# Kernel optimization log

Hardware: AMD Instinct MI355X
Metric: run time of the kernel (lower is better)

The kernel has to match this reference:

```python
import jax, jax.numpy as jnp
import numpy as np

K = 5
PAD = 2


def setup_inputs() -> dict:
    key = jax.random.key(0)
    k1, k2 = jax.random.split(key)
    B, C, H, W = 8, 4, 256, 256
    x = jax.random.normal(k1, (B, C, H, W), dtype=jnp.float32)
    filt = jax.random.uniform(k2, (B, C * K * K, H, W), dtype=jnp.float32)
    return {"x": x, "filt": filt}


def reference(x, filt):
    B, C, H, W = x.shape
    # identity kernel: out channel j of each group picks the j-th position of the kxk window
    eye = jnp.eye(K * K, dtype=x.dtype).reshape(K * K, 1, K, K)
    kernel = jnp.tile(eye, (C, 1, 1, 1))  # [C*K^2, 1, K, K], grouped conv = per-channel patch expand
    x_localexpand = jax.lax.conv_general_dilated(
        x, kernel,
        window_strides=(1, 1),
        padding=[(PAD, PAD), (PAD, PAD)],
        dimension_numbers=("NCHW", "OIHW", "NCHW"),
        feature_group_count=C,
    )  # [B, C*K^2, H, W]
    y = jnp.tanh(jnp.sum(x_localexpand * filt, axis=1, keepdims=True))  # [B,1,H,W]
    return y
```

## Files before the change

kernel.cpp:

```cpp
#include <hip/hip_runtime.h>
#include <math.h>

#define Hd 256
#define Wd 256
#define Cc 4
#define KK 5
#define HT 8
#define XWR (HT + KK - 1)

typedef float v4f __attribute__((ext_vector_type(4)));

#define GLD16(gaddr, laddr)                                                          \
    __builtin_amdgcn_global_load_lds(                                                \
        (const __attribute__((address_space(1))) void*)(gaddr),                      \
        (__attribute__((address_space(3))) void*)(laddr), 16, 0, 0)

__global__ __launch_bounds__(256, 1) void dynf_kernel(const float* __restrict__ x,
                                                      const float* __restrict__ filt,
                                                      float* __restrict__ out) {
    const int bid  = blockIdx.x;
    const int lg   = ((bid & 7) << 5) + (bid >> 3);
    const int b    = lg >> 5;
    const int h0   = (lg & 31) << 3;
    const int c    = threadIdx.x >> 6;
    const int lane = threadIdx.x & 63;
    const int w0   = lane << 2;

    const size_t HW = (size_t)Hd * Wd;

    __shared__ float lds[2][Cc][HT][Wd];

    const float* xc = x + ((size_t)b * Cc + c) * HW;
    const float* fb = filt + ((size_t)b * (Cc * KK * KK) + (size_t)c * (KK * KK)) * HW
                      + (size_t)h0 * Wd + w0;
    float* l0 = &lds[0][c][0][0];
    float* l1 = &lds[1][c][0][0];

    float xw[XWR][8];
    const v4f vz = {0.f, 0.f, 0.f, 0.f};
#pragma unroll
    for (int ri = 0; ri < XWR; ++ri) {
        const int g = h0 + ri - 2;
        if (g >= 0 && g < Hd) {
            const float* xr = xc + (size_t)g * Wd;
            v4f left  = *(const v4f*)(xr + (w0 ? (w0 - 4) : 0));
            v4f mid   = *(const v4f*)(xr + w0);
            v4f right = *(const v4f*)(xr + ((w0 + 4 < Wd) ? (w0 + 4) : 0));
            if (w0 == 0)      left  = vz;
            if (w0 + 4 >= Wd) right = vz;
            xw[ri][0] = left.z;  xw[ri][1] = left.w;
            xw[ri][2] = mid.x;   xw[ri][3] = mid.y;
            xw[ri][4] = mid.z;   xw[ri][5] = mid.w;
            xw[ri][6] = right.x; xw[ri][7] = right.y;
        } else {
#pragma unroll
            for (int j = 0; j < 8; ++j) xw[ri][j] = 0.f;
        }
    }

#pragma unroll
    for (int r = 0; r < HT; ++r) GLD16(fb + (size_t)r * Wd, l0 + r * Wd);
    asm volatile("" ::: "memory");
#pragma unroll
    for (int r = 0; r < HT; ++r) GLD16(fb + HW + (size_t)r * Wd, l1 + r * Wd);
    asm volatile("" ::: "memory");

    v4f acc[HT];
#pragma unroll
    for (int r = 0; r < HT; ++r) acc[r] = vz;

#pragma unroll
    for (int p = 0; p < KK * KK; ++p) {
        if (p < KK * KK - 1) asm volatile("s_waitcnt vmcnt(8)" ::: "memory");
        else                 asm volatile("s_waitcnt vmcnt(0)" ::: "memory");

        const int di = p / KK, dj = p % KK;
        const float* ls = (p & 1) ? l1 : l0;
#pragma unroll
        for (int r = 0; r < HT; ++r) {
            v4f f = *(const v4f*)(ls + r * Wd + w0);
            acc[r].x = fmaf(xw[r + di][0 + dj], f.x, acc[r].x);
            acc[r].y = fmaf(xw[r + di][1 + dj], f.y, acc[r].y);
            acc[r].z = fmaf(xw[r + di][2 + dj], f.z, acc[r].z);
            acc[r].w = fmaf(xw[r + di][3 + dj], f.w, acc[r].w);
        }

        if (p + 2 < KK * KK) {
            asm volatile("s_waitcnt lgkmcnt(0)" ::: "memory");
            float* ld = (p & 1) ? l1 : l0;
#pragma unroll
            for (int r = 0; r < HT; ++r)
                GLD16(fb + (size_t)(p + 2) * HW + (size_t)r * Wd, ld + r * Wd);
            asm volatile("" ::: "memory");
        }
    }

    __syncthreads();
    v4f* red = (v4f*)&lds[0][0][0][0];
#pragma unroll
    for (int r = 0; r < HT; ++r) red[(c * HT + r) * 64 + lane] = acc[r];
    __syncthreads();

#pragma unroll
    for (int rr = 0; rr < 2; ++rr) {
        const int r = c * 2 + rr;
        v4f s = red[(0 * HT + r) * 64 + lane] + red[(1 * HT + r) * 64 + lane]
              + red[(2 * HT + r) * 64 + lane] + red[(3 * HT + r) * 64 + lane];
        v4f o;
        o.x = tanhf(s.x); o.y = tanhf(s.y); o.z = tanhf(s.z); o.w = tanhf(s.w);
        __builtin_nontemporal_store(o, (v4f*)(out + (size_t)b * HW + (size_t)(h0 + r) * Wd + w0));
    }
}

extern "C" void kernel_launch(void* const* d_in, const int* in_sizes, int n_in,
                              void* d_out, int out_size, void* d_ws, size_t ws_size,
                              hipStream_t stream) {
    const float* x    = (const float*)d_in[0];
    const float* filt = (const float*)d_in[1];
    float* out        = (float*)d_out;

    const int grid  = 256;
    const int block = 256;
    dynf_kernel<<<grid, block, 0, stream>>>(x, filt, out);
}
```

Baseline: 337.5 us.

## Replace LDS double-buffered filter pipeline with direct nontemporal loads and smaller tiles

Removes the global-to-LDS async double buffering of the filter and reads filter vectors directly into registers with nontemporal loads. The row tile shrinks from 8 to 4 rows, the grid doubles to 512 blocks, and launch bounds allow two blocks per CU. This aims to expose more independent loads and more resident waves to saturate HBM bandwidth, removing waitcnt-serialized pipeline stages. The cost is more redundant halo loads of x per output row and reliance on the compiler to schedule the loads.

Result: faster. 277.7 us (-17.7%).

```diff
diff --git a/kernel.cpp b/kernel.cpp
--- a/kernel.cpp
+++ b/kernel.cpp
@@ -5,36 +5,26 @@
 #define Wd 256
 #define Cc 4
 #define KK 5
-#define HT 8
+#define HT 4
 #define XWR (HT + KK - 1)
 
 typedef float v4f __attribute__((ext_vector_type(4)));
 
-#define GLD16(gaddr, laddr)                                                          \
-    __builtin_amdgcn_global_load_lds(                                                \
-        (const __attribute__((address_space(1))) void*)(gaddr),                      \
-        (__attribute__((address_space(3))) void*)(laddr), 16, 0, 0)
-
-__global__ __launch_bounds__(256, 1) void dynf_kernel(const float* __restrict__ x,
+__global__ __launch_bounds__(256, 2) void dynf_kernel(const float* __restrict__ x,
                                                       const float* __restrict__ filt,
                                                       float* __restrict__ out) {
     const int bid  = blockIdx.x;
-    const int lg   = ((bid & 7) << 5) + (bid >> 3);
-    const int b    = lg >> 5;
-    const int h0   = (lg & 31) << 3;
+    const int lg   = ((bid & 7) << 6) + (bid >> 3);
+    const int b    = lg >> 6;
+    const int h0   = (lg & 63) << 2;
     const int c    = threadIdx.x >> 6;
     const int lane = threadIdx.x & 63;
     const int w0   = lane << 2;
 
     const size_t HW = (size_t)Hd * Wd;
-
-    __shared__ float lds[2][Cc][HT][Wd];
-
     const float* xc = x + ((size_t)b * Cc + c) * HW;
     const float* fb = filt + ((size_t)b * (Cc * KK * KK) + (size_t)c * (KK * KK)) * HW
                       + (size_t)h0 * Wd + w0;
-    float* l0 = &lds[0][c][0][0];
-    float* l1 = &lds[1][c][0][0];
 
     float xw[XWR][8];
     const v4f vz = {0.f, 0.f, 0.f, 0.f};
@@ -58,54 +48,32 @@
         }
     }
 
-#pragma unroll
-    for (int r = 0; r < HT; ++r) GLD16(fb + (size_t)r * Wd, l0 + r * Wd);
-    asm volatile("" ::: "memory");
-#pragma unroll
-    for (int r = 0; r < HT; ++r) GLD16(fb + HW + (size_t)r * Wd, l1 + r * Wd);
-    asm volatile("" ::: "memory");
-
     v4f acc[HT];
 #pragma unroll
     for (int r = 0; r < HT; ++r) acc[r] = vz;
 
 #pragma unroll
     for (int p = 0; p < KK * KK; ++p) {
-        if (p < KK * KK - 1) asm volatile("s_waitcnt vmcnt(8)" ::: "memory");
-        else                 asm volatile("s_waitcnt vmcnt(0)" ::: "memory");
-
         const int di = p / KK, dj = p % KK;
-        const float* ls = (p & 1) ? l1 : l0;
+        const float* fp = fb + (size_t)p * HW;
 #pragma unroll
         for (int r = 0; r < HT; ++r) {
-            v4f f = *(const v4f*)(ls + r * Wd + w0);
+            v4f f = __builtin_nontemporal_load((const v4f*)(fp + (size_t)r * Wd));
             acc[r].x = fmaf(xw[r + di][0 + dj], f.x, acc[r].x);
             acc[r].y = fmaf(xw[r + di][1 + dj], f.y, acc[r].y);
             acc[r].z = fmaf(xw[r + di][2 + dj], f.z, acc[r].z);
             acc[r].w = fmaf(xw[r + di][3 + dj], f.w, acc[r].w);
         }
-
-        if (p + 2 < KK * KK) {
-            asm volatile("s_waitcnt lgkmcnt(0)" ::: "memory");
-            float* ld = (p & 1) ? l1 : l0;
-#pragma unroll
-            for (int r = 0; r < HT; ++r)
-                GLD16(fb + (size_t)(p + 2) * HW + (size_t)r * Wd, ld + r * Wd);
-            asm volatile("" ::: "memory");
-        }
     }
 
-    __syncthreads();
-    v4f* red = (v4f*)&lds[0][0][0][0];
+    __shared__ v4f red[Cc][HT][64];
 #pragma unroll
-    for (int r = 0; r < HT; ++r) red[(c * HT + r) * 64 + lane] = acc[r];
+    for (int r = 0; r < HT; ++r) red[c][r][lane] = acc[r];
     __syncthreads();
 
-#pragma unroll
-    for (int rr = 0; rr < 2; ++rr) {
-        const int r = c * 2 + rr;
-        v4f s = red[(0 * HT + r) * 64 + lane] + red[(1 * HT + r) * 64 + lane]
-              + red[(2 * HT + r) * 64 + lane] + red[(3 * HT + r) * 64 + lane];
+    {
+        const int r = c;
+        v4f s = red[0][r][lane] + red[1][r][lane] + red[2][r][lane] + red[3][r][lane];
         v4f o;
         o.x = tanhf(s.x); o.y = tanhf(s.y); o.z = tanhf(s.z); o.w = tanhf(s.w);
         __builtin_nontemporal_store(o, (v4f*)(out + (size_t)b * HW + (size_t)(h0 + r) * Wd + w0));
@@ -119,7 +87,7 @@
     const float* filt = (const float*)d_in[1];
     float* out        = (float*)d_out;
 
-    const int grid  = 256;
+    const int grid  = 512;
     const int block = 256;
     dynf_kernel<<<grid, block, 0, stream>>>(x, filt, out);
 }
```
